# Kernel tuning notes

Hardware: AMD Instinct MI355X
Metric: run time of the kernel (lower is better)

## Reference

```python
import jax, jax.numpy as jnp
import numpy as np

EMBED_DIM = 2048
NUM_HEADS = 16
HEAD_DIM = EMBED_DIM // NUM_HEADS
SCALES = [(1, 1, 1), (1, 2, 2), (1, 4, 4), (1, 6, 6), (1, 8, 8),
          (1, 12, 12), (1, 16, 16), (1, 20, 20), (1, 24, 24), (1, 32, 32)]
LENS = [t * h * w for (t, h, w) in SCALES]
SEQ_LEN = int(np.sum(LENS))  # 2521
BATCH = 2
MAX_SCALE_MUL = float(np.log(100.0))


def _block_causal_bias():
    # VAR-style: queries in scale-block i attend to all keys up to end of block i.
    cum = np.cumsum(LENS)
    q_end = np.repeat(cum, LENS)                      # [L] visible kv length per query
    visible = np.arange(SEQ_LEN)[None, :] < q_end[:, None]
    bias = np.where(visible, 0.0, -np.inf).astype(np.float32)
    return jnp.asarray(bias)[None, None]              # [1,1,L,L]


def setup_inputs() -> dict:
    key = jax.random.key(0)
    ks = jax.random.split(key, 8)
    C, H, hd, L, B = EMBED_DIM, NUM_HEADS, HEAD_DIM, SEQ_LEN, BATCH
    x = jax.random.normal(ks[0], (B, L, C), dtype=jnp.float32)
    W_qkv = jax.random.normal(ks[1], (3 * C, C), dtype=jnp.float32) * (1.0 / np.sqrt(C))
    q_bias = jnp.zeros((C,), jnp.float32)
    v_bias = jnp.zeros((C,), jnp.float32)
    scale_mul_log = jnp.full((1, H, 1, 1), np.log(4.0), jnp.float32)
    proj_W = jax.random.normal(ks[2], (C, C), dtype=jnp.float32) * (1.0 / np.sqrt(C))
    proj_b = jnp.zeros((C,), jnp.float32)
    # 2D RoPE cache, pre-sliced for scale_ind=0: (2,1,1,1,L,hd//2) = (cos, sin)
    angles = jax.random.uniform(ks[3], (L, hd // 2), dtype=jnp.float32, maxval=2.0 * np.pi)
    rope_cache = jnp.stack([jnp.cos(angles), jnp.sin(angles)])[:, None, None, None]
    attn_bias = _block_causal_bias()
    return {"x": x, "W_qkv": W_qkv, "q_bias": q_bias, "v_bias": v_bias,
            "scale_mul_log": scale_mul_log, "proj_W": proj_W, "proj_b": proj_b,
            "rope_cache": rope_cache, "attn_bias": attn_bias}


def _l2norm(t, eps=1e-12):
    # torch F.normalize: x / max(||x||_2, eps)
    n = jnp.sqrt(jnp.sum(t * t, axis=-1, keepdims=True))
    return t / jnp.maximum(n, eps)


def reference(x, W_qkv, q_bias, v_bias, scale_mul_log, proj_W, proj_b, rope_cache, attn_bias):
    B, L, C = x.shape
    H, hd = NUM_HEADS, HEAD_DIM
    bias = jnp.concatenate([q_bias, jnp.zeros_like(q_bias), v_bias])
    qkv = x @ W_qkv.T + bias                               # [B,L,3C]
    qkv = qkv.reshape(B, L, 3, H, hd).transpose(2, 0, 3, 1, 4)  # [3,B,H,L,hd]
    q, k, v = qkv[0], qkv[1], qkv[2]
    # cosine attention: L2-norm q,k; q scaled by clamped learnable per-head scale
    scale_mul = jnp.exp(jnp.minimum(scale_mul_log, MAX_SCALE_MUL))
    q = _l2norm(q) * scale_mul
    k = _l2norm(k)
    # 2D RoPE applied jointly to q and k
    qk = jnp.stack([q, k]).reshape(2, B, H, L, hd // 2, 2)
    cos, sin = rope_cache[0], rope_cache[1]                # [1,1,1,L,hd//2]
    re = cos * qk[..., 0] - sin * qk[..., 1]
    im = sin * qk[..., 0] + cos * qk[..., 1]
    qk = jnp.stack([re, im], axis=-1).reshape(2, B, H, L, hd)
    q, k = qk[0], qk[1]
    # SDPA with scale=1 (cos_attn) and additive block-causal bias
    scores = jnp.einsum('bhqd,bhkd->bhqk', q, k) + attn_bias
    attn = jax.nn.softmax(scores, axis=-1)
    out = jnp.einsum('bhqk,bhkd->bhqd', attn, v)           # [B,H,L,hd]
    out = out.transpose(0, 2, 1, 3).reshape(B, L, C)
    return out @ proj_W.T + proj_b
```

## Files before the change

kernel.cpp:

```cpp
#include <hip/hip_runtime.h>
#include <stdint.h>

#define SEQL 2521
#define LPAD 2560
#define NB 2
#define NH 16
#define HD 128
#define CD 2048
#define KD 2048

typedef float f32x4 __attribute__((ext_vector_type(4)));
typedef __bf16 bf16x8 __attribute__((ext_vector_type(8)));
typedef unsigned short u16x8 __attribute__((ext_vector_type(8)));

static __device__ __forceinline__ unsigned short bf16c(float f){
  __bf16 h = (__bf16)f;
  return __builtin_bit_cast(unsigned short, h);
}
static __device__ __forceinline__ float bf2f(unsigned short s){
  union { unsigned u; float f; } v; v.u = ((unsigned)s) << 16; return v.f;
}
static __device__ __forceinline__ bf16x8 asbf(u16x8 v){ return __builtin_bit_cast(bf16x8, v); }

typedef const __attribute__((address_space(1))) unsigned int* gas1_t;
typedef __attribute__((address_space(3))) unsigned int* las3_t;
static __device__ __forceinline__ void glds16(const void* g, void* l){
  __builtin_amdgcn_global_load_lds((gas1_t)g, (las3_t)l, 16, 0, 0);
}

__global__ __launch_bounds__(256) void prep_kernel(
    const float* __restrict__ x, const float* __restrict__ wqkv, const float* __restrict__ projw,
    unsigned short* __restrict__ xb, unsigned short* __restrict__ wb, unsigned short* __restrict__ pw)
{
  const int NX = (NB*LPAD*CD)/4;
  const int NW = (3*CD*CD)/4;
  const int NPj = (CD*CD)/4;
  const int total = NX + NW + NPj;
  for (int v = blockIdx.x*256 + threadIdx.x; v < total; v += gridDim.x*256){
    if (v < NX){
      int e = v << 2;
      int row = e >> 11, col = e & 2047;
      int b = (row >= LPAD) ? 1 : 0;
      int l = row - b*LPAD;
      ushort4 o;
      if (l < SEQL){
        const float4 f = *(const float4*)(x + (((long)(b*SEQL + l)) << 11) + col);
        o.x = bf16c(f.x); o.y = bf16c(f.y); o.z = bf16c(f.z); o.w = bf16c(f.w);
      } else { o.x = 0; o.y = 0; o.z = 0; o.w = 0; }
      *(ushort4*)(xb + e) = o;
    } else if (v < NX + NW){
      long i = (long)(v - NX) << 2;
      const float4 f = *(const float4*)(wqkv + i);
      ushort4 o; o.x=bf16c(f.x); o.y=bf16c(f.y); o.z=bf16c(f.z); o.w=bf16c(f.w);
      *(ushort4*)(wb + i) = o;
    } else {
      long i = (long)(v - NX - NW) << 2;
      const float4 f = *(const float4*)(projw + i);
      ushort4 o; o.x=bf16c(f.x); o.y=bf16c(f.y); o.z=bf16c(f.z); o.w=bf16c(f.w);
      *(ushort4*)(pw + i) = o;
    }
  }
}

static __device__ __forceinline__ void gemm8p(
    const unsigned short* __restrict__ A, const unsigned short* __restrict__ Bm,
    unsigned short* lds, int m0, int n0, f32x4 acc[8][4])
{
  const int tid = threadIdx.x;
  const int w = tid >> 6, lane = tid & 63;
  const int g = lane >> 4, lr = lane & 15;
  const int wm = w >> 2, wn = w & 3;
  const int xorv = (lr & 7) << 3;
  const int off0 = (g << 3) ^ xorv;
  const int arow = wm*128 + lr;
  const int brow = wn*64 + lr;

  auto stage = [&](int mat, int kt, int half, int buf){
    const unsigned short* G = mat ? Bm : A;
    const int base0 = mat ? n0 : m0;
    unsigned short* lb = lds + buf*32768 + mat*16384;
#pragma unroll
    for (int p = 0; p < 2; ++p){
      const int cb_ = (half<<10) + (p<<9) + (w<<6);
      const int c = cb_ + lane;
      const int row = c >> 3, cc = c & 7;
      glds16(G + (size_t)(base0 + row)*KD + (kt<<6) + ((cc ^ (row & 7)) << 3),
             lb + (cb_ << 3));
    }
  };
  auto rdA = [&](int buf, int i, int ks)->u16x8 {
    return *(const u16x8*)(lds + buf*32768 + (arow + i*16)*64 + (off0 ^ (ks<<5)));
  };
  auto rdB = [&](int buf, int j, int ks)->u16x8 {
    return *(const u16x8*)(lds + buf*32768 + 16384 + (brow + j*16)*64 + (off0 ^ (ks<<5)));
  };

  u16x8 bfr[4][2], af[2][2];
  auto mfma16 = [&](int q){
#pragma unroll
    for (int i2 = 0; i2 < 2; ++i2)
#pragma unroll
      for (int ks = 0; ks < 2; ++ks)
#pragma unroll
        for (int j = 0; j < 4; ++j)
          acc[2*q+i2][j] = __builtin_amdgcn_mfma_f32_16x16x32_bf16(
              asbf(af[i2][ks]), asbf(bfr[j][ks]), acc[2*q+i2][j], 0, 0, 0);
  };

#define PH_SYNC_MFMA(Q) \
    __builtin_amdgcn_s_barrier(); \
    asm volatile("s_waitcnt lgkmcnt(0)" ::: "memory"); \
    __builtin_amdgcn_s_setprio(1); mfma16(Q); __builtin_amdgcn_s_setprio(0);

  stage(0, 0, 0, 0); stage(0, 0, 1, 0);
  stage(1, 0, 0, 0); stage(1, 0, 1, 0);
  stage(1, 1, 0, 1); stage(1, 1, 1, 1);
  asm volatile("s_waitcnt vmcnt(4)" ::: "memory");
  __builtin_amdgcn_s_barrier();

  const int NI = KD >> 7;
  for (int it = 0; it < NI; ++it){
    const int kt = it << 1;
    const bool last = (it == NI-1);
#pragma unroll
    for (int j = 0; j < 4; ++j){ bfr[j][0]=rdB(0,j,0); bfr[j][1]=rdB(0,j,1); }
    af[0][0]=rdA(0,0,0); af[0][1]=rdA(0,0,1); af[1][0]=rdA(0,1,0); af[1][1]=rdA(0,1,1);
    stage(0, kt+1, 0, 1);
    PH_SYNC_MFMA(0)
    __builtin_amdgcn_s_barrier();

    af[0][0]=rdA(0,2,0); af[0][1]=rdA(0,2,1); af[1][0]=rdA(0,3,0); af[1][1]=rdA(0,3,1);
    stage(0, kt+1, 1, 1);
    PH_SYNC_MFMA(1)
    __builtin_amdgcn_s_barrier();

    af[0][0]=rdA(0,4,0); af[0][1]=rdA(0,4,1); af[1][0]=rdA(0,5,0); af[1][1]=rdA(0,5,1);
    if (!last) stage(1, kt+2, 0, 0);
    PH_SYNC_MFMA(2)
    __builtin_amdgcn_s_barrier();

    af[0][0]=rdA(0,6,0); af[0][1]=rdA(0,6,1); af[1][0]=rdA(0,7,0); af[1][1]=rdA(0,7,1);
    if (!last) stage(1, kt+2, 1, 0);
    PH_SYNC_MFMA(3)
    if (last) { asm volatile("s_waitcnt vmcnt(0)" ::: "memory"); }
    else      { asm volatile("s_waitcnt vmcnt(4)" ::: "memory"); }
    __builtin_amdgcn_s_barrier();

#pragma unroll
    for (int j = 0; j < 4; ++j){ bfr[j][0]=rdB(1,j,0); bfr[j][1]=rdB(1,j,1); }
    af[0][0]=rdA(1,0,0); af[0][1]=rdA(1,0,1); af[1][0]=rdA(1,1,0); af[1][1]=rdA(1,1,1);
    if (!last) stage(0, kt+2, 0, 0);
    PH_SYNC_MFMA(0)
    __builtin_amdgcn_s_barrier();

    af[0][0]=rdA(1,2,0); af[0][1]=rdA(1,2,1); af[1][0]=rdA(1,3,0); af[1][1]=rdA(1,3,1);
    if (!last) stage(0, kt+2, 1, 0);
    PH_SYNC_MFMA(1)
    __builtin_amdgcn_s_barrier();

    af[0][0]=rdA(1,4,0); af[0][1]=rdA(1,4,1); af[1][0]=rdA(1,5,0); af[1][1]=rdA(1,5,1);
    if (!last) stage(1, kt+3, 0, 1);
    PH_SYNC_MFMA(2)
    __builtin_amdgcn_s_barrier();

    af[0][0]=rdA(1,6,0); af[0][1]=rdA(1,6,1); af[1][0]=rdA(1,7,0); af[1][1]=rdA(1,7,1);
    if (!last) stage(1, kt+3, 1, 1);
    PH_SYNC_MFMA(3)
    if (last) { asm volatile("s_waitcnt vmcnt(0)" ::: "memory"); }
    else      { asm volatile("s_waitcnt vmcnt(4)" ::: "memory"); }
    __builtin_amdgcn_s_barrier();
  }
#undef PH_SYNC_MFMA
}

__global__ __launch_bounds__(512, 2) void gemm_qkv(
    const unsigned short* __restrict__ A, const unsigned short* __restrict__ W,
    const float* __restrict__ qb, const float* __restrict__ vb,
    unsigned short* __restrict__ qg, unsigned short* __restrict__ kg,
    unsigned short* __restrict__ vt)
{
  __shared__ __align__(16) unsigned short lds[65536];
  f32x4 acc[8][4] = {};
  const int bid = blockIdx.x;
  const int swz = (bid & 7)*60 + (bid >> 3);
  const int mt = swz / 24, ntt = swz % 24;
  const int m0 = mt << 8, n0 = ntt << 8;
  gemm8p(A, W, lds, m0, n0, acc);

  const int tid = threadIdx.x;
  const int w = tid >> 6, lane = tid & 63, g = lane >> 4, lr = lane & 15;
  const int wm = w >> 2, wn = w & 3;
  const int part = n0 >> 11;
  const int b = (m0 >= LPAD) ? 1 : 0;
  const int l0 = m0 - b*LPAD;
  const int colbase = (n0 & 2047) + wn*64;
#pragma unroll
  for (int i = 0; i < 8; ++i){
    const int mloc = wm*128 + i*16 + (g << 2);
#pragma unroll
    for (int j = 0; j < 4; ++j){
      const int col = colbase + j*16 + lr;
      const int hb = col >> 7, d = col & 127;
      const float bias = (part == 0) ? qb[col] : ((part == 2) ? vb[col] : 0.f);
      const f32x4 v = acc[i][j];
      if (part == 2){
        ushort4 o;
        o.x = bf16c(v[0] + bias); o.y = bf16c(v[1] + bias);
        o.z = bf16c(v[2] + bias); o.w = bf16c(v[3] + bias);
        *(ushort4*)(vt + ((size_t)((b*NH + hb)*HD + d))*LPAD + l0 + mloc) = o;
      } else {
        unsigned short* dst = (part ? kg : qg) + (((size_t)(b*NH + hb)*LPAD) + l0 + mloc)*HD + d;
        dst[0]     = bf16c(v[0] + bias);
        dst[HD]    = bf16c(v[1] + bias);
        dst[2*HD]  = bf16c(v[2] + bias);
        dst[3*HD]  = bf16c(v[3] + bias);
      }
    }
  }
}

__global__ __launch_bounds__(512, 2) void gemm_proj(
    const unsigned short* __restrict__ A, const unsigned short* __restrict__ W,
    const float* __restrict__ pbias, float* __restrict__ out)
{
  __shared__ __align__(16) unsigned short lds[65536];
  f32x4 acc[8][4] = {};
  const int bid = blockIdx.x;
  const int swz = (bid & 7)*20 + (bid >> 3);
  const int mt = swz >> 3, ntt = swz & 7;
  const int m0 = mt << 8, n0 = ntt << 8;
  gemm8p(A, W, lds, m0, n0, acc);

  const int tid = threadIdx.x;
  const int w = tid >> 6, lane = tid & 63, g = lane >> 4, lr = lane & 15;
  const int wm = w >> 2, wn = w & 3;
  const int b = (m0 >= LPAD) ? 1 : 0;
  const int l0 = m0 - b*LPAD;
#pragma unroll
  for (int i = 0; i < 8; ++i){
    const int mloc = wm*128 + i*16 + (g << 2);
#pragma unroll
    for (int j = 0; j < 4; ++j){
      const int n = n0 + wn*64 + j*16 + lr;
      const float bias = pbias[n];
      const f32x4 v = acc[i][j];
#pragma unroll
      for (int r = 0; r < 4; ++r){
        const int l = l0 + mloc + r;
        if (l < SEQL) out[(((size_t)(b*SEQL + l)) << 11) + n] = v[r] + bias;
      }
    }
  }
}

__global__ __launch_bounds__(256) void rope_norm(
    unsigned short* __restrict__ qg, unsigned short* __restrict__ kg,
    const float* __restrict__ rope, const float* __restrict__ smlog)
{
  const int sub = threadIdx.x & 15;
  const int l = blockIdx.x*16 + (threadIdx.x >> 4);
  if (l >= SEQL) return;
  const int pb = blockIdx.y;
  const int part = pb >> 5, bh = pb & 31, h = bh & 15;
  unsigned short* base = (part ? kg : qg) + ((long)bh*LPAD + l)*HD + (sub << 3);
  const u16x8 v = *(const u16x8*)base;
  float f[8];
#pragma unroll
  for (int i = 0; i < 8; ++i) f[i] = bf2f(v[i]);
  float ss = 0.f;
#pragma unroll
  for (int i = 0; i < 8; ++i) ss += f[i]*f[i];
  ss += __shfl_xor(ss, 1, 16);
  ss += __shfl_xor(ss, 2, 16);
  ss += __shfl_xor(ss, 4, 16);
  ss += __shfl_xor(ss, 8, 16);
  float inv = 1.f / fmaxf(sqrtf(ss), 1e-12f);
  if (part == 0){
    float sl = fminf(smlog[h], 4.605170185988091f);
    inv *= __expf(sl) * 1.4426950408889634f;
  }
  const float4 cs = *(const float4*)(rope + (long)l*64 + (sub << 2));
  const float4 sn = *(const float4*)(rope + (long)(SEQL + l)*64 + (sub << 2));
  u16x8 o;
  const float c4[4] = {cs.x, cs.y, cs.z, cs.w};
  const float s4[4] = {sn.x, sn.y, sn.z, sn.w};
#pragma unroll
  for (int p = 0; p < 4; ++p){
    const float re = f[2*p], im = f[2*p+1];
    o[2*p]   = bf16c((c4[p]*re - s4[p]*im)*inv);
    o[2*p+1] = bf16c((s4[p]*re + c4[p]*im)*inv);
  }
  *(u16x8*)base = o;
}

static __device__ __forceinline__ int q_end_of(int q){
  if (q >= SEQL) return 1;
  if (q < 121){
    if (q < 1) return 1;
    if (q < 5) return 5;
    if (q < 21) return 21;
    if (q < 57) return 57;
    return 121;
  }
  if (q < 265) return 265;
  if (q < 521) return 521;
  if (q < 921) return 921;
  if (q < 1497) return 1497;
  return 2521;
}

__global__ __launch_bounds__(512) void attn_kernel(
    const unsigned short* __restrict__ qg, const unsigned short* __restrict__ kg,
    const unsigned short* __restrict__ vt, unsigned short* __restrict__ aout)
{
  __shared__ __align__(16) unsigned short Ks[64*128];
  __shared__ __align__(16) unsigned short Vs[128*64];
  __shared__ __align__(16) unsigned short Ps[8][16*72];
  const int tid = threadIdx.x, w = tid >> 6, lane = tid & 63;
  const int g = lane >> 4, lr = lane & 15;
  const int qt = (int)gridDim.x - 1 - (int)blockIdx.x;
  const int bh = blockIdx.y;
  const int q0 = qt << 7, qw = q0 + (w << 4);
  const long kvBase = (long)bh * LPAD * HD;

  u16x8 qf[4];
  {
    const unsigned short* qrow = qg + kvBase + (long)(qw + lr)*HD + (g << 3);
#pragma unroll
    for (int c = 0; c < 4; ++c) qf[c] = *(const u16x8*)(qrow + (c << 5));
  }
  const int qe  = q_end_of(qw + lr);
  const int qe0 = q_end_of(qw);
  const int qmax = (q0 + 127 < SEQL - 1) ? q0 + 127 : SEQL - 1;
  const int nt = (q_end_of(qmax) + 63) >> 6;

  float m2 = -1e30f, l_run = 0.f;
  f32x4 acco[8] = {};

  for (int t = 0; t < nt; ++t){
    __syncthreads();
    const int kvb = t << 6;
#pragma unroll
    for (int c = 0; c < 2; ++c){
      const int idx = (c << 9) + tid;
      const int kv = idx >> 4, ch = idx & 15;
      glds16(kg + kvBase + (long)(kvb + kv)*HD + ((ch ^ (kv & 7)) << 3),
             Ks + (c << 12) + (w << 9));
      const int dd = idx >> 3, ch2 = idx & 7;
      glds16(vt + kvBase + (long)dd*LPAD + kvb + ((ch2 ^ (dd & 7)) << 3),
             Vs + (c << 12) + (w << 9));
    }
    __syncthreads();

    f32x4 accs[4] = {};
    __builtin_amdgcn_s_setprio(1);
#pragma unroll
    for (int mf = 0; mf < 4; ++mf){
      const int kvr = (mf << 4) + lr;
      const unsigned short* krow = Ks + kvr*HD;
      const int sw = kvr & 7;
#pragma unroll
      for (int c = 0; c < 4; ++c){
        u16x8 kf = *(const u16x8*)(krow + ((((c << 2) + g) ^ sw) << 3));
        accs[mf] = __builtin_amdgcn_mfma_f32_16x16x32_bf16(asbf(kf), asbf(qf[c]), accs[mf], 0, 0, 0);
      }
    }
    __builtin_amdgcn_s_setprio(0);

    float tmax = -1e30f;
    if (kvb + 64 <= qe0){
#pragma unroll
      for (int mf = 0; mf < 4; ++mf)
#pragma unroll
        for (int r = 0; r < 4; ++r) tmax = fmaxf(tmax, accs[mf][r]);
    } else {
#pragma unroll
      for (int mf = 0; mf < 4; ++mf){
#pragma unroll
        for (int r = 0; r < 4; ++r){
          const int kvg = kvb + (mf << 4) + (g << 2) + r;
          float s = (kvg < qe) ? accs[mf][r] : -1e30f;
          accs[mf][r] = s;
          tmax = fmaxf(tmax, s);
        }
      }
    }
    tmax = fmaxf(tmax, __shfl_xor(tmax, 16, 64));
    tmax = fmaxf(tmax, __shfl_xor(tmax, 32, 64));

    float alpha = 1.f;
    const bool need = !__all(tmax <= m2 + 11.0f);
    if (need){
      const float mnew = fmaxf(m2, tmax);
      alpha = exp2f(m2 - mnew);
      m2 = mnew;
      const float a0 = __shfl(alpha, (g << 2) + 0, 64);
      const float a1 = __shfl(alpha, (g << 2) + 1, 64);
      const float a2 = __shfl(alpha, (g << 2) + 2, 64);
      const float a3 = __shfl(alpha, (g << 2) + 3, 64);
#pragma unroll
      for (int nf = 0; nf < 8; ++nf){
        acco[nf][0] *= a0; acco[nf][1] *= a1; acco[nf][2] *= a2; acco[nf][3] *= a3;
      }
    }

    float tsum = 0.f;
#pragma unroll
    for (int mf = 0; mf < 4; ++mf){
#pragma unroll
      for (int r = 0; r < 4; ++r){
        const float p = exp2f(accs[mf][r] - m2);
        accs[mf][r] = p;
        tsum += p;
      }
    }
    tsum += __shfl_xor(tsum, 16, 64);
    tsum += __shfl_xor(tsum, 32, 64);
    l_run = l_run*alpha + tsum;

    unsigned short* prow = &Ps[w][lr*72 + (g << 2)];
#pragma unroll
    for (int mf = 0; mf < 4; ++mf){
      uint2 pk;
      pk.x = (unsigned)bf16c(accs[mf][0]) | ((unsigned)bf16c(accs[mf][1]) << 16);
      pk.y = (unsigned)bf16c(accs[mf][2]) | ((unsigned)bf16c(accs[mf][3]) << 16);
      *(uint2*)(prow + (mf << 4)) = pk;
    }

    __builtin_amdgcn_s_setprio(1);
#pragma unroll
    for (int c = 0; c < 2; ++c){
      u16x8 pf = *(const u16x8*)(&Ps[w][lr*72 + (c << 5) + (g << 3)]);
      const int sw2 = lr & 7;
#pragma unroll
      for (int nf = 0; nf < 8; ++nf){
        u16x8 vf = *(const u16x8*)(Vs + ((nf << 4) + lr)*64 + ((((c << 2) + g) ^ sw2) << 3));
        acco[nf] = __builtin_amdgcn_mfma_f32_16x16x32_bf16(asbf(pf), asbf(vf), acco[nf], 0, 0, 0);
      }
    }
    __builtin_amdgcn_s_setprio(0);
  }

  const float rcp = 1.f / l_run;
  const float li0 = __shfl(rcp, (g << 2) + 0, 64);
  const float li1 = __shfl(rcp, (g << 2) + 1, 64);
  const float li2 = __shfl(rcp, (g << 2) + 2, 64);
  const float li3 = __shfl(rcp, (g << 2) + 3, 64);
  const int b = bh >> 4, h = bh & 15;
#pragma unroll
  for (int r = 0; r < 4; ++r){
    const int qq = qw + (g << 2) + r;
    if (qq < SEQL){
      const float lir = (r == 0) ? li0 : ((r == 1) ? li1 : ((r == 2) ? li2 : li3));
      unsigned short* dst = aout + (((long)(b*LPAD + qq)) << 11) + (h << 7) + lr;
#pragma unroll
      for (int nf = 0; nf < 8; ++nf)
        dst[nf << 4] = bf16c(acco[nf][r] * lir);
    }
  }
}

extern "C" void kernel_launch(void* const* d_in, const int* in_sizes, int n_in,
                              void* d_out, int out_size, void* d_ws, size_t ws_size,
                              hipStream_t stream) {
  const float* x     = (const float*)d_in[0];
  const float* wqkv  = (const float*)d_in[1];
  const float* qb    = (const float*)d_in[2];
  const float* vb    = (const float*)d_in[3];
  const float* smlog = (const float*)d_in[4];
  const float* projw = (const float*)d_in[5];
  const float* projb = (const float*)d_in[6];
  const float* rope  = (const float*)d_in[7];
  float* out = (float*)d_out;

  unsigned short* xb = (unsigned short*)d_ws;
  unsigned short* wb = xb + (size_t)NB*LPAD*CD;
  unsigned short* pw = wb + (size_t)3*CD*CD;
  unsigned short* qg = pw + (size_t)CD*CD;
  unsigned short* kg = qg + (size_t)NB*NH*LPAD*HD;
  unsigned short* vt = kg + (size_t)NB*NH*LPAD*HD;

  prep_kernel<<<2048, 256, 0, stream>>>(x, wqkv, projw, xb, wb, pw);
  gemm_qkv<<<480, 512, 0, stream>>>(xb, wb, qb, vb, qg, kg, vt);
  rope_norm<<<dim3(158, 64), 256, 0, stream>>>(qg, kg, rope, smlog);
  attn_kernel<<<dim3(20, 32), 512, 0, stream>>>(qg, kg, vt, xb);
  gemm_proj<<<160, 512, 0, stream>>>(xb, pw, projb, out);
}
```

Before: 535.3 us.

## Restructure attention: 4 waves x 32 rows, double-buffered KV, register P

Attention blocks now use 256 threads with each wave handling two 16-row query slices, so every K/V fragment read from LDS feeds two MFMAs. K/V tiles are double-buffered, with the next tile staged asynchronously before computing the current one, and explicit waitcnt/barriers replace __syncthreads. The P matrix is kept in registers by permuting the K row order in the QK^T MFMA so its output matches the PV operand layout, which removes the Ps LDS round-trip. Register pressure roughly doubles per wave, which may reduce occupancy.

```diff
diff --git a/kernel.cpp b/kernel.cpp
--- a/kernel.cpp
+++ b/kernel.cpp
@@ -309,153 +309,196 @@
   return 2521;
 }
 
-__global__ __launch_bounds__(512) void attn_kernel(
+__global__ __launch_bounds__(256, 2) void attn_kernel(
     const unsigned short* __restrict__ qg, const unsigned short* __restrict__ kg,
     const unsigned short* __restrict__ vt, unsigned short* __restrict__ aout)
 {
-  __shared__ __align__(16) unsigned short Ks[64*128];
-  __shared__ __align__(16) unsigned short Vs[128*64];
-  __shared__ __align__(16) unsigned short Ps[8][16*72];
+  __shared__ __align__(16) unsigned short Ks[2*64*128];
+  __shared__ __align__(16) unsigned short Vs[2*128*64];
   const int tid = threadIdx.x, w = tid >> 6, lane = tid & 63;
-  const int g = lane >> 4, lr = lane & 15;
+  const int g = lane >> 4, lr = lane & 15, lr7 = lr & 7;
   const int qt = (int)gridDim.x - 1 - (int)blockIdx.x;
   const int bh = blockIdx.y;
-  const int q0 = qt << 7, qw = q0 + (w << 4);
+  const int q0 = qt << 7, qw = q0 + (w << 5);
   const long kvBase = (long)bh * LPAD * HD;
 
-  u16x8 qf[4];
+  u16x8 qfA[4], qfB[4];
   {
     const unsigned short* qrow = qg + kvBase + (long)(qw + lr)*HD + (g << 3);
 #pragma unroll
-    for (int c = 0; c < 4; ++c) qf[c] = *(const u16x8*)(qrow + (c << 5));
-  }
-  const int qe  = q_end_of(qw + lr);
+    for (int c = 0; c < 4; ++c) qfA[c] = *(const u16x8*)(qrow + (c << 5));
+    const unsigned short* qrow2 = qrow + (long)16*HD;
+#pragma unroll
+    for (int c = 0; c < 4; ++c) qfB[c] = *(const u16x8*)(qrow2 + (c << 5));
+  }
+  const int qeA = q_end_of(qw + lr);
+  const int qeB = q_end_of(qw + 16 + lr);
   const int qe0 = q_end_of(qw);
   const int qmax = (q0 + 127 < SEQL - 1) ? q0 + 127 : SEQL - 1;
   const int nt = (q_end_of(qmax) + 63) >> 6;
 
-  float m2 = -1e30f, l_run = 0.f;
-  f32x4 acco[8] = {};
+  float m2A = -1e30f, lA = 0.f, m2B = -1e30f, lB = 0.f;
+  f32x4 oA[8] = {}, oB[8] = {};
+
+  auto stageKV = [&](int t, int buf){
+    const int kvb2 = t << 6;
+#pragma unroll
+    for (int c = 0; c < 4; ++c){
+      const int cb = (c << 8) + tid;
+      const int row = cb >> 4, cc = cb & 15;
+      const int fk = (row & 3) | (((row >> 3) & 1) << 2);
+      const int sc = (cc & 8) | ((cc & 7) ^ fk);
+      glds16(kg + kvBase + (size_t)(kvb2 + row)*HD + (sc << 3),
+             Ks + buf*8192 + (((c << 8) + (w << 6)) << 3));
+    }
+#pragma unroll
+    for (int c = 0; c < 4; ++c){
+      const int cb = (c << 8) + tid;
+      const int d = cb >> 3, cc = cb & 7;
+      const int sc = cc ^ (d & 7);
+      glds16(vt + kvBase + (size_t)d*LPAD + kvb2 + (sc << 3),
+             Vs + buf*8192 + (((c << 8) + (w << 6)) << 3));
+    }
+  };
+
+  stageKV(0, 0);
 
   for (int t = 0; t < nt; ++t){
-    __syncthreads();
+    __builtin_amdgcn_s_barrier();
+    const bool pf = (t + 1 < nt);
+    if (pf){
+      stageKV(t + 1, (t + 1) & 1);
+      asm volatile("s_waitcnt vmcnt(8)" ::: "memory");
+    } else {
+      asm volatile("s_waitcnt vmcnt(0)" ::: "memory");
+    }
+    __builtin_amdgcn_s_barrier();
+
+    const unsigned short* Kb = Ks + (t & 1)*8192;
+    const unsigned short* Vb = Vs + (t & 1)*8192;
     const int kvb = t << 6;
+
+    f32x4 sA[4] = {}, sB[4] = {};
+    __builtin_amdgcn_s_setprio(1);
+#pragma unroll
+    for (int mf = 0; mf < 4; ++mf){
+      const int kvr = ((mf & 1) << 2) + ((mf >> 1) << 5) + ((lr >> 2) << 3) + (lr & 3);
+      const unsigned short* kr = Kb + kvr*HD;
+#pragma unroll
+      for (int c = 0; c < 4; ++c){
+        const int cc = (c << 2) + g;
+        const int swz = (cc & 8) | ((cc & 7) ^ lr7);
+        const u16x8 kf = *(const u16x8*)(kr + (swz << 3));
+        sA[mf] = __builtin_amdgcn_mfma_f32_16x16x32_bf16(asbf(kf), asbf(qfA[c]), sA[mf], 0, 0, 0);
+        sB[mf] = __builtin_amdgcn_mfma_f32_16x16x32_bf16(asbf(kf), asbf(qfB[c]), sB[mf], 0, 0, 0);
+      }
+    }
+    __builtin_amdgcn_s_setprio(0);
+
+    const bool fullvis = (kvb + 64 <= qe0);
+
+#define SM_STEP(SS, M2, LL, OO, QEL, ALPHA) { \
+    float tmax = -1e30f; \
+    if (fullvis){ \
+      _Pragma("unroll") for (int mf = 0; mf < 4; ++mf) \
+        _Pragma("unroll") for (int r = 0; r < 4; ++r) tmax = fmaxf(tmax, SS[mf][r]); \
+    } else { \
+      _Pragma("unroll") for (int mf = 0; mf < 4; ++mf){ \
+        _Pragma("unroll") for (int r = 0; r < 4; ++r){ \
+          const int kvg = kvb + (g << 3) + ((mf & 1) << 2) + r + ((mf >> 1) << 5); \
+          float s_ = (kvg < QEL) ? SS[mf][r] : -1e30f; \
+          SS[mf][r] = s_; tmax = fmaxf(tmax, s_); \
+        } \
+      } \
+    } \
+    tmax = fmaxf(tmax, __shfl_xor(tmax, 16, 64)); \
+    tmax = fmaxf(tmax, __shfl_xor(tmax, 32, 64)); \
+    float ALPHA = 1.f; \
+    if (!__all(tmax <= M2 + 11.0f)){ \
+      const float mnew = fmaxf(M2, tmax); \
+      ALPHA = exp2f(M2 - mnew); M2 = mnew; \
+      const float a0 = __shfl(ALPHA, (g << 2) + 0, 64); \
+      const float a1 = __shfl(ALPHA, (g << 2) + 1, 64); \
+      const float a2 = __shfl(ALPHA, (g << 2) + 2, 64); \
+      const float a3 = __shfl(ALPHA, (g << 2) + 3, 64); \
+      _Pragma("unroll") for (int nf = 0; nf < 8; ++nf){ \
+        OO[nf][0] *= a0; OO[nf][1] *= a1; OO[nf][2] *= a2; OO[nf][3] *= a3; \
+      } \
+    } \
+    float ts = 0.f; \
+    _Pragma("unroll") for (int mf = 0; mf < 4; ++mf){ \
+      _Pragma("unroll") for (int r = 0; r < 4; ++r){ \
+        const float p_ = exp2f(SS[mf][r] - M2); SS[mf][r] = p_; ts += p_; \
+      } \
+    } \
+    ts += __shfl_xor(ts, 16, 64); \
+    ts += __shfl_xor(ts, 32, 64); \
+    LL = LL*ALPHA + ts; }
+
+    SM_STEP(sA, m2A, lA, oA, qeA, alphaA)
+    SM_STEP(sB, m2B, lB, oB, qeB, alphaB)
+#undef SM_STEP
+
+    u16x8 paA[2], paB[2];
 #pragma unroll
     for (int c = 0; c < 2; ++c){
-      const int idx = (c << 9) + tid;
-      const int kv = idx >> 4, ch = idx & 15;
-      glds16(kg + kvBase + (long)(kvb + kv)*HD + ((ch ^ (kv & 7)) << 3),
-             Ks + (c << 12) + (w << 9));
-      const int dd = idx >> 3, ch2 = idx & 7;
-      glds16(vt + kvBase + (long)dd*LPAD + kvb + ((ch2 ^ (dd & 7)) << 3),
-             Vs + (c << 12) + (w << 9));
-    }
-    __syncthreads();
-
-    f32x4 accs[4] = {};
+#pragma unroll
+      for (int r = 0; r < 4; ++r){
+        paA[c][r]   = bf16c(sA[2*c][r]);
+        paA[c][4+r] = bf16c(sA[2*c+1][r]);
+        paB[c][r]   = bf16c(sB[2*c][r]);
+        paB[c][4+r] = bf16c(sB[2*c+1][r]);
+      }
+    }
+
     __builtin_amdgcn_s_setprio(1);
 #pragma unroll
-    for (int mf = 0; mf < 4; ++mf){
-      const int kvr = (mf << 4) + lr;
-      const unsigned short* krow = Ks + kvr*HD;
-      const int sw = kvr & 7;
-#pragma unroll
-      for (int c = 0; c < 4; ++c){
-        u16x8 kf = *(const u16x8*)(krow + ((((c << 2) + g) ^ sw) << 3));
-        accs[mf] = __builtin_amdgcn_mfma_f32_16x16x32_bf16(asbf(kf), asbf(qf[c]), accs[mf], 0, 0, 0);
+    for (int c = 0; c < 2; ++c){
+#pragma unroll
+      for (int nf = 0; nf < 8; ++nf){
+        const u16x8 vf = *(const u16x8*)(Vb + ((nf << 4) + lr)*64 + ((((c << 2) + g) ^ lr7) << 3));
+        oA[nf] = __builtin_amdgcn_mfma_f32_16x16x32_bf16(asbf(paA[c]), asbf(vf), oA[nf], 0, 0, 0);
+        oB[nf] = __builtin_amdgcn_mfma_f32_16x16x32_bf16(asbf(paB[c]), asbf(vf), oB[nf], 0, 0, 0);
       }
     }
     __builtin_amdgcn_s_setprio(0);
-
-    float tmax = -1e30f;
-    if (kvb + 64 <= qe0){
-#pragma unroll
-      for (int mf = 0; mf < 4; ++mf)
-#pragma unroll
-        for (int r = 0; r < 4; ++r) tmax = fmaxf(tmax, accs[mf][r]);
-    } else {
-#pragma unroll
-      for (int mf = 0; mf < 4; ++mf){
-#pragma unroll
-        for (int r = 0; r < 4; ++r){
-          const int kvg = kvb + (mf << 4) + (g << 2) + r;
-          float s = (kvg < qe) ? accs[mf][r] : -1e30f;
-          accs[mf][r] = s;
-          tmax = fmaxf(tmax, s);
-        }
-      }
-    }
-    tmax = fmaxf(tmax, __shfl_xor(tmax, 16, 64));
-    tmax = fmaxf(tmax, __shfl_xor(tmax, 32, 64));
-
-    float alpha = 1.f;
-    const bool need = !__all(tmax <= m2 + 11.0f);
-    if (need){
-      const float mnew = fmaxf(m2, tmax);
-      alpha = exp2f(m2 - mnew);
-      m2 = mnew;
-      const float a0 = __shfl(alpha, (g << 2) + 0, 64);
-      const float a1 = __shfl(alpha, (g << 2) + 1, 64);
-      const float a2 = __shfl(alpha, (g << 2) + 2, 64);
-      const float a3 = __shfl(alpha, (g << 2) + 3, 64);
-#pragma unroll
-      for (int nf = 0; nf < 8; ++nf){
-        acco[nf][0] *= a0; acco[nf][1] *= a1; acco[nf][2] *= a2; acco[nf][3] *= a3;
-      }
-    }
-
-    float tsum = 0.f;
-#pragma unroll
-    for (int mf = 0; mf < 4; ++mf){
-#pragma unroll
-      for (int r = 0; r < 4; ++r){
-        const float p = exp2f(accs[mf][r] - m2);
-        accs[mf][r] = p;
-        tsum += p;
-      }
-    }
-    tsum += __shfl_xor(tsum, 16, 64);
-    tsum += __shfl_xor(tsum, 32, 64);
-    l_run = l_run*alpha + tsum;
-
-    unsigned short* prow = &Ps[w][lr*72 + (g << 2)];
-#pragma unroll
-    for (int mf = 0; mf < 4; ++mf){
-      uint2 pk;
-      pk.x = (unsigned)bf16c(accs[mf][0]) | ((unsigned)bf16c(accs[mf][1]) << 16);
-      pk.y = (unsigned)bf16c(accs[mf][2]) | ((unsigned)bf16c(accs[mf][3]) << 16);
-      *(uint2*)(prow + (mf << 4)) = pk;
-    }
-
-    __builtin_amdgcn_s_setprio(1);
-#pragma unroll
-    for (int c = 0; c < 2; ++c){
-      u16x8 pf = *(const u16x8*)(&Ps[w][lr*72 + (c << 5) + (g << 3)]);
-      const int sw2 = lr & 7;
-#pragma unroll
-      for (int nf = 0; nf < 8; ++nf){
-        u16x8 vf = *(const u16x8*)(Vs + ((nf << 4) + lr)*64 + ((((c << 2) + g) ^ sw2) << 3));
-        acco[nf] = __builtin_amdgcn_mfma_f32_16x16x32_bf16(asbf(pf), asbf(vf), acco[nf], 0, 0, 0);
-      }
-    }
-    __builtin_amdgcn_s_setprio(0);
-  }
-
-  const float rcp = 1.f / l_run;
-  const float li0 = __shfl(rcp, (g << 2) + 0, 64);
-  const float li1 = __shfl(rcp, (g << 2) + 1, 64);
-  const float li2 = __shfl(rcp, (g << 2) + 2, 64);
-  const float li3 = __shfl(rcp, (g << 2) + 3, 64);
+  }
+
   const int b = bh >> 4, h = bh & 15;
-#pragma unroll
-  for (int r = 0; r < 4; ++r){
-    const int qq = qw + (g << 2) + r;
-    if (qq < SEQL){
-      const float lir = (r == 0) ? li0 : ((r == 1) ? li1 : ((r == 2) ? li2 : li3));
-      unsigned short* dst = aout + (((long)(b*LPAD + qq)) << 11) + (h << 7) + lr;
-#pragma unroll
-      for (int nf = 0; nf < 8; ++nf)
-        dst[nf << 4] = bf16c(acco[nf][r] * lir);
+  {
+    const float rcp = 1.f / lA;
+    const float li0 = __shfl(rcp, (g << 2) + 0, 64);
+    const float li1 = __shfl(rcp, (g << 2) + 1, 64);
+    const float li2 = __shfl(rcp, (g << 2) + 2, 64);
+    const float li3 = __shfl(rcp, (g << 2) + 3, 64);
+#pragma unroll
+    for (int r = 0; r < 4; ++r){
+      const int qq = qw + (g << 2) + r;
+      if (qq < SEQL){
+        const float lir = (r == 0) ? li0 : ((r == 1) ? li1 : ((r == 2) ? li2 : li3));
+        unsigned short* dst = aout + (((long)(b*LPAD + qq)) << 11) + (h << 7) + lr;
+#pragma unroll
+        for (int nf = 0; nf < 8; ++nf)
+          dst[nf << 4] = bf16c(oA[nf][r] * lir);
+      }
+    }
+  }
+  {
+    const float rcp = 1.f / lB;
+    const float li0 = __shfl(rcp, (g << 2) + 0, 64);
+    const float li1 = __shfl(rcp, (g << 2) + 1, 64);
+    const float li2 = __shfl(rcp, (g << 2) + 2, 64);
+    const float li3 = __shfl(rcp, (g << 2) + 3, 64);
+#pragma unroll
+    for (int r = 0; r < 4; ++r){
+      const int qq = qw + 16 + (g << 2) + r;
+      if (qq < SEQL){
+        const float lir = (r == 0) ? li0 : ((r == 1) ? li1 : ((r == 2) ? li2 : li3));
+        unsigned short* dst = aout + (((long)(b*LPAD + qq)) << 11) + (h << 7) + lr;
+#pragma unroll
+        for (int nf = 0; nf < 8; ++nf)
+          dst[nf << 4] = bf16c(oB[nf][r] * lir);
+      }
     }
   }
 }
@@ -483,6 +526,6 @@
   prep_kernel<<<2048, 256, 0, stream>>>(x, wqkv, projw, xb, wb, pw);
   gemm_qkv<<<480, 512, 0, stream>>>(xb, wb, qb, vb, qg, kg, vt);
   rope_norm<<<dim3(158, 64), 256, 0, stream>>>(qg, kg, rope, smlog);
-  attn_kernel<<<dim3(20, 32), 512, 0, stream>>>(qg, kg, vt, xb);
+  attn_kernel<<<dim3(20, 32), 256, 0, stream>>>(qg, kg, vt, xb);
   gemm_proj<<<160, 512, 0, stream>>>(xb, pw, projb, out);
 }
```

Measured after the change: 525.1 us. About the same (-1.9%).
